# Performance work log

Measured on AMD Instinct MI355X. Metric: run time of the kernel, lower is better.

The kernel has to match this reference:

```python
import jax, jax.numpy as jnp
import numpy as np

N = 100000
E = 640000
WIDTH = 128
NUM_FEATURES = 64


def _linear_relu(h, W, b):
    # LinearBlock with batch_norm=False, dropout=0.0 -> Linear + ReLU
    return jax.nn.relu(h @ W + b)


def setup_inputs() -> dict:
    key = jax.random.key(0)
    k = jax.random.split(key, 8)
    x = jax.random.normal(k[0], (N, WIDTH), dtype=jnp.float32)
    e = jax.random.randint(k[1], (2, E), 0, N, dtype=jnp.int32)
    e_feat = jax.random.normal(k[2], (E, NUM_FEATURES), dtype=jnp.float32)
    s_e = 1.0 / np.sqrt(WIDTH + NUM_FEATURES)
    s_m = 1.0 / np.sqrt(2 * WIDTH)
    W_edge = jax.random.uniform(k[3], (WIDTH + NUM_FEATURES, WIDTH), jnp.float32, -s_e, s_e)
    b_edge = jax.random.uniform(k[4], (WIDTH,), jnp.float32, -s_e, s_e)
    W_mlp = jax.random.uniform(k[5], (2 * WIDTH, WIDTH), jnp.float32, -s_m, s_m)
    b_mlp = jax.random.uniform(k[6], (WIDTH,), jnp.float32, -s_m, s_m)
    return {"x": x, "e": e, "e_feat": e_feat, "W_edge": W_edge, "b_edge": b_edge,
            "W_mlp": W_mlp, "b_mlp": b_mlp}


def reference(x, e, e_feat, W_edge, b_edge, W_mlp, b_mlp):
    src, dst = e[0], e[1]
    diffs = x[dst] - x[src]                                   # [E, width]
    ef = diffs + _linear_relu(jnp.concatenate([diffs, e_feat], axis=1), W_edge, b_edge)
    maxes = jax.ops.segment_max(ef, dst, num_segments=x.shape[0])  # [N, width]
    # torch_scatter.scatter_max leaves empty segments at 0
    maxes = jnp.where(jnp.isneginf(maxes), 0.0, maxes)
    return x + _linear_relu(jnp.concatenate([x, maxes], axis=1), W_mlp, b_mlp)
```

## Files before the change

kernel.cpp:

```cpp
#include <hip/hip_runtime.h>
#include <hip/hip_bf16.h>
#include <limits.h>

#define NNODES 100000
#define NEDGES 640000
#define WIDTH  128
#define NFEAT  64
#define KA     192
#define KA_PAD 196
#define KB     256
#define KB_PAD 264
#define MT     64
#define STC    68
#define NB_SCAN ((NNODES + 255) / 256)
#define NB_HIST ((NEDGES + 255) / 256)
#define NB_PREP (((KA + KB) * WIDTH + 255) / 256)

typedef __attribute__((ext_vector_type(8))) short short8;
typedef __attribute__((ext_vector_type(4))) short short4v;
typedef __attribute__((ext_vector_type(4))) float floatx4;

__device__ __forceinline__ short f2bf_rne(float f) {
    unsigned u = __float_as_uint(f);
    unsigned r = u + 0x7fffu + ((u >> 16) & 1u);
    return (short)(r >> 16);
}
__device__ __forceinline__ short f2bf_t(float f) {
    return (short)(__float_as_uint(f) >> 16);
}
__device__ __forceinline__ float bf2f(short s) {
    return __uint_as_float(((unsigned)(unsigned short)s) << 16);
}
__device__ __forceinline__ unsigned encu(float f) {
    unsigned u = __float_as_uint(f);
    return (u & 0x80000000u) ? ~u : (u | 0x80000000u);
}
__device__ __forceinline__ float decu(unsigned e) {
    unsigned u = (e & 0x80000000u) ? (e ^ 0x80000000u) : ~e;
    return __uint_as_float(u);
}

__global__ __launch_bounds__(256) void prep_hist_kernel(
    const int* __restrict__ e, int* __restrict__ counts,
    const float* __restrict__ W_edge, const float* __restrict__ W_mlp,
    short* __restrict__ We_t, short* __restrict__ Wm_t)
{
    int b = blockIdx.x;
    if (b < NB_HIST) {
        int i = b * 256 + threadIdx.x;
        if (i < NEDGES) atomicAdd(&counts[e[NEDGES + i]], 1);
    } else {
        int t = (b - NB_HIST) * 256 + threadIdx.x;
        if (t < KA * WIDTH) {
            int k = t / WIDTH, n = t % WIDTH;
            We_t[n * KA + k] = f2bf_rne(W_edge[t]);
        } else if (t < (KA + KB) * WIDTH) {
            int j = t - KA * WIDTH;
            int k = j / WIDTH, n = j % WIDTH;
            Wm_t[n * KB + k] = f2bf_rne(W_mlp[j]);
        }
    }
}

__global__ __launch_bounds__(256) void scanA_kernel(
    const int* __restrict__ counts, int* __restrict__ cursor, int* __restrict__ blockSum)
{
    __shared__ int s[256];
    int tid = threadIdx.x;
    int n = blockIdx.x * 256 + tid;
    int c = (n < NNODES) ? counts[n] : 0;
    s[tid] = c;
    __syncthreads();
    for (int off = 1; off < 256; off <<= 1) {
        int v = (tid >= off) ? s[tid - off] : 0;
        __syncthreads();
        s[tid] += v;
        __syncthreads();
    }
    if (n < NNODES) cursor[n] = s[tid] - c;
    if (tid == 255) blockSum[blockIdx.x] = s[255];
}

__global__ __launch_bounds__(512) void scanB_kernel(int* __restrict__ blockSum,
                                                    int* __restrict__ blockOff)
{
    __shared__ int s[512];
    int tid = threadIdx.x;
    int c = (tid < NB_SCAN) ? blockSum[tid] : 0;
    s[tid] = c;
    __syncthreads();
    for (int off = 1; off < 512; off <<= 1) {
        int v = (tid >= off) ? s[tid - off] : 0;
        __syncthreads();
        s[tid] += v;
        __syncthreads();
    }
    if (tid < NB_SCAN) blockOff[tid] = s[tid] - c;
}

__global__ __launch_bounds__(256) void scatter_kernel(
    const int* __restrict__ e, int* __restrict__ cursor,
    const int* __restrict__ blockOff,
    uint2* __restrict__ pSD, int* __restrict__ pEid)
{
    int i = blockIdx.x * 256 + threadIdx.x;
    if (i < NEDGES) {
        int s = e[i];
        int d = e[NEDGES + i];
        int p = atomicAdd(&cursor[d], 1) + blockOff[d >> 8];
        pSD[p] = make_uint2((unsigned)s, (unsigned)d);
        pEid[p] = i;
    }
}

__global__ __launch_bounds__(256, 6) void edge_kernel(
    const float* __restrict__ x, const float* __restrict__ e_feat,
    const short* __restrict__ We_t, const float* __restrict__ b_edge,
    const uint2* __restrict__ pSD, const int* __restrict__ pEid,
    unsigned* __restrict__ mEnc)
{
    __shared__ __align__(16) short sA[MT * KA_PAD];
    __shared__ float sBias[WIDTH];
    __shared__ int   sDst[MT];
    __shared__ int   sHeadRow[MT + 1];
    __shared__ int   sMeta[3];

    const int tid = threadIdx.x;
    if (tid < WIDTH) sBias[tid] = b_edge[tid];

    const int bid = blockIdx.x;
    const int btile = (bid & 7) * (NEDGES / MT / 8) + (bid >> 3);
    const int e0 = btile * MT;

    const float4* xf4 = (const float4*)x;
    const float4* ef4 = (const float4*)e_feat;

    {
        int mq = tid >> 5, c = tid & 31;
        uint2 sd[8];
        #pragma unroll
        for (int j = 0; j < 8; ++j) sd[j] = pSD[e0 + mq + 8 * j];
        int mq2 = tid >> 4, c2 = tid & 15;
        int eid[4];
        #pragma unroll
        for (int j = 0; j < 4; ++j) eid[j] = pEid[e0 + mq2 + 16 * j];

        float4 xsA[4], xdA[4];
        #pragma unroll
        for (int j = 0; j < 4; ++j) {
            xsA[j] = xf4[(size_t)sd[j].x * 32 + c];
            xdA[j] = xf4[(size_t)sd[j].y * 32 + c];
        }
        float4 xsB[4], xdB[4];
        #pragma unroll
        for (int j = 0; j < 4; ++j) {
            xsB[j] = xf4[(size_t)sd[4 + j].x * 32 + c];
            xdB[j] = xf4[(size_t)sd[4 + j].y * 32 + c];
        }
        if (c == 0) {
            #pragma unroll
            for (int j = 0; j < 8; ++j) sDst[mq + 8 * j] = (int)sd[j].y;
        }
        #pragma unroll
        for (int j = 0; j < 4; ++j) {
            int mm = mq + 8 * j;
            short4v df;
            df.x = f2bf_t(xdA[j].x - xsA[j].x);
            df.y = f2bf_t(xdA[j].y - xsA[j].y);
            df.z = f2bf_t(xdA[j].z - xsA[j].z);
            df.w = f2bf_t(xdA[j].w - xsA[j].w);
            *(short4v*)&sA[mm * KA_PAD + c * 4] = df;
        }
        float4 fv[4];
        #pragma unroll
        for (int j = 0; j < 4; ++j) fv[j] = ef4[(size_t)eid[j] * 16 + c2];
        #pragma unroll
        for (int j = 0; j < 4; ++j) {
            int mm = mq + 8 * (4 + j);
            short4v df;
            df.x = f2bf_t(xdB[j].x - xsB[j].x);
            df.y = f2bf_t(xdB[j].y - xsB[j].y);
            df.z = f2bf_t(xdB[j].z - xsB[j].z);
            df.w = f2bf_t(xdB[j].w - xsB[j].w);
            *(short4v*)&sA[mm * KA_PAD + c * 4] = df;
        }
        #pragma unroll
        for (int j = 0; j < 4; ++j) {
            int mm = mq2 + 16 * j;
            short4v sv;
            sv.x = f2bf_t(fv[j].x); sv.y = f2bf_t(fv[j].y);
            sv.z = f2bf_t(fv[j].z); sv.w = f2bf_t(fv[j].w);
            *(short4v*)&sA[mm * KA_PAD + WIDTH + c2 * 4] = sv;
        }
    }
    __syncthreads();

    if (tid < 64) {
        bool head = (tid == 0) || (sDst[tid] != sDst[tid - 1]);
        unsigned long long mask = __ballot(head);
        int rank = __popcll(mask & ((1ull << tid) - 1ull));
        if (head) sHeadRow[rank] = tid;
        if (tid == 0) {
            int nh = (int)__popcll(mask);
            sMeta[0] = nh;
            sHeadRow[nh] = MT;
            int prevSame = 0, nextSame = 0;
            if (e0 > 0)           prevSame = (pSD[e0 - 1].y  == (unsigned)sDst[0]);
            if (e0 + MT < NEDGES) nextSame = (pSD[e0 + MT].y == (unsigned)sDst[MT - 1]);
            sMeta[1] = prevSame; sMeta[2] = nextSame;
        }
    }

    const int wave = tid >> 6;
    const int lane = tid & 63;
    const int l15  = lane & 15;
    const int kq   = (lane >> 4) << 3;
    const int quad = lane >> 4;

    floatx4 acc[4][2];
    #pragma unroll
    for (int rt = 0; rt < 4; ++rt)
        #pragma unroll
        for (int ct = 0; ct < 2; ++ct)
            acc[rt][ct] = (floatx4){0.f, 0.f, 0.f, 0.f};

    #pragma unroll
    for (int kc = 0; kc < 6; ++kc) {
        int k0 = kc * 32 + kq;
        short8 a[4];
        #pragma unroll
        for (int rt = 0; rt < 4; ++rt)
            a[rt] = *(const short8*)&sA[(rt * 16 + l15) * KA_PAD + k0];
        short8 b[2];
        #pragma unroll
        for (int ct = 0; ct < 2; ++ct)
            b[ct] = *(const short8*)&We_t[(size_t)(wave * 32 + ct * 16 + l15) * KA + k0];
        #pragma unroll
        for (int rt = 0; rt < 4; ++rt)
            #pragma unroll
            for (int ct = 0; ct < 2; ++ct)
                acc[rt][ct] = __builtin_amdgcn_mfma_f32_16x16x32_bf16(a[rt], b[ct], acc[rt][ct], 0, 0, 0);
    }

    #pragma unroll
    for (int rt = 0; rt < 4; ++rt) {
        #pragma unroll
        for (int ct = 0; ct < 2; ++ct) {
            int col = wave * 32 + ct * 16 + l15;
            float bias = sBias[col];
            #pragma unroll
            for (int i = 0; i < 4; ++i) {
                int row = rt * 16 + quad * 4 + i;
                float v = acc[rt][ct][i] + bias;
                v = v > 0.f ? v : 0.f;
                acc[rt][ct][i] = v + bf2f(sA[row * KA_PAD + col]);
            }
        }
    }
    __syncthreads();

    short* sT = sA;
    #pragma unroll
    for (int rt = 0; rt < 4; ++rt) {
        #pragma unroll
        for (int ct = 0; ct < 2; ++ct) {
            int col = wave * 32 + ct * 16 + l15;
            short4v pk;
            pk.x = f2bf_t(acc[rt][ct][0]);
            pk.y = f2bf_t(acc[rt][ct][1]);
            pk.z = f2bf_t(acc[rt][ct][2]);
            pk.w = f2bf_t(acc[rt][ct][3]);
            *(short4v*)&sT[col * STC + rt * 16 + quad * 4] = pk;
        }
    }
    __syncthreads();

    const int nh = sMeta[0], prevSame = sMeta[1], nextSame = sMeta[2];
    const unsigned* sT32 = (const unsigned*)sT;
    for (int p = tid; p < (nh << 7); p += 256) {
        int h = p >> 7, c = p & 127;
        int r0 = sHeadRow[h], r1 = sHeadRow[h + 1];
        const unsigned* colp = sT32 + c * (STC / 2);
        int w0 = r0 >> 1, w1 = (r1 - 1) >> 1;
        float m = -3.4e38f;
        for (int w = w0; w <= w1; ++w) {
            unsigned u = colp[w];
            float flo = bf2f((short)(u & 0xffffu));
            float fhi = bf2f((short)(u >> 16));
            if (2 * w >= r0)    m = fmaxf(m, flo);
            if (2 * w + 1 < r1) m = fmaxf(m, fhi);
        }
        int dst = sDst[r0];
        unsigned ev = encu(m);
        unsigned* dp = &mEnc[(size_t)dst * WIDTH + c];
        bool atom = (h == 0 && prevSame) || (h == nh - 1 && nextSame);
        if (atom) atomicMax(dp, ev);
        else      *dp = ev;
    }
}

__global__ __launch_bounds__(256) void node_kernel(
    const float* __restrict__ x, const short* __restrict__ Wm_t,
    const float* __restrict__ b_mlp, float* __restrict__ out)
{
    __shared__ short sA[MT * KB_PAD];
    __shared__ float sBias[WIDTH];

    const int tid = threadIdx.x;
    if (tid < WIDTH) sBias[tid] = b_mlp[tid];

    const int n0 = blockIdx.x * MT;
    const float4* xf4 = (const float4*)x;
    const uint4* enc4 = (const uint4*)out;

    {
        int mq = tid >> 5, c = tid & 31;
        #pragma unroll
        for (int mm = mq; mm < MT; mm += 8) {
            int node = n0 + mm;
            if (node >= NNODES) node = NNODES - 1;
            float4 xv = xf4[(size_t)node * 32 + c];
            short4v sx;
            sx.x = f2bf_rne(xv.x); sx.y = f2bf_rne(xv.y);
            sx.z = f2bf_rne(xv.z); sx.w = f2bf_rne(xv.w);
            *(short4v*)&sA[mm * KB_PAD + c * 4] = sx;
            uint4 ev = enc4[(size_t)node * 32 + c];
            short4v sm;
            sm.x = f2bf_rne(ev.x == 0u ? 0.f : decu(ev.x));
            sm.y = f2bf_rne(ev.y == 0u ? 0.f : decu(ev.y));
            sm.z = f2bf_rne(ev.z == 0u ? 0.f : decu(ev.z));
            sm.w = f2bf_rne(ev.w == 0u ? 0.f : decu(ev.w));
            *(short4v*)&sA[mm * KB_PAD + WIDTH + c * 4] = sm;
        }
    }
    __syncthreads();

    const int wave = tid >> 6;
    const int lane = tid & 63;
    const int l15  = lane & 15;
    const int kq   = (lane >> 4) << 3;
    const int quad = lane >> 4;

    floatx4 acc[4][2];
    #pragma unroll
    for (int rt = 0; rt < 4; ++rt)
        #pragma unroll
        for (int ct = 0; ct < 2; ++ct)
            acc[rt][ct] = (floatx4){0.f, 0.f, 0.f, 0.f};

    #pragma unroll
    for (int kc = 0; kc < 8; ++kc) {
        int k0 = kc * 32 + kq;
        short8 a[4];
        #pragma unroll
        for (int rt = 0; rt < 4; ++rt)
            a[rt] = *(const short8*)&sA[(rt * 16 + l15) * KB_PAD + k0];
        short8 b[2];
        #pragma unroll
        for (int ct = 0; ct < 2; ++ct)
            b[ct] = *(const short8*)&Wm_t[(size_t)(wave * 32 + ct * 16 + l15) * KB + k0];
        #pragma unroll
        for (int rt = 0; rt < 4; ++rt)
            #pragma unroll
            for (int ct = 0; ct < 2; ++ct)
                acc[rt][ct] = __builtin_amdgcn_mfma_f32_16x16x32_bf16(a[rt], b[ct], acc[rt][ct], 0, 0, 0);
    }

    #pragma unroll
    for (int rt = 0; rt < 4; ++rt) {
        #pragma unroll
        for (int ct = 0; ct < 2; ++ct) {
            int col = wave * 32 + ct * 16 + l15;
            float bias = sBias[col];
            #pragma unroll
            for (int i = 0; i < 4; ++i) {
                int row = rt * 16 + quad * 4 + i;
                int node = n0 + row;
                if (node < NNODES) {
                    float v = acc[rt][ct][i] + bias;
                    v = v > 0.f ? v : 0.f;
                    out[(size_t)node * WIDTH + col] = x[(size_t)node * WIDTH + col] + v;
                }
            }
        }
    }
}

extern "C" void kernel_launch(void* const* d_in, const int* in_sizes, int n_in,
                              void* d_out, int out_size, void* d_ws, size_t ws_size,
                              hipStream_t stream) {
    const float* x      = (const float*)d_in[0];
    const int*   e      = (const int*)d_in[1];
    const float* e_feat = (const float*)d_in[2];
    const float* W_edge = (const float*)d_in[3];
    const float* b_edge = (const float*)d_in[4];
    const float* W_mlp  = (const float*)d_in[5];
    const float* b_mlp  = (const float*)d_in[6];
    float*    out  = (float*)d_out;
    unsigned* mEnc = (unsigned*)d_out;

    short* We_t = (short*)d_ws;
    short* Wm_t = We_t + (size_t)KA * WIDTH;
    int* base     = (int*)((char*)d_ws + 114688);
    uint2* pSD    = (uint2*)base;
    int* pEid     = (int*)(base + 2 * NEDGES);
    int* counts   = pEid + NEDGES;
    int* cursor   = counts + NNODES;
    int* blockSum = cursor + NNODES;
    int* blockOff = blockSum + NB_SCAN;

    hipMemsetAsync(d_out, 0, (size_t)NNODES * WIDTH * 4, stream);
    hipMemsetAsync(counts, 0, (size_t)NNODES * 4, stream);
    prep_hist_kernel<<<NB_HIST + NB_PREP, 256, 0, stream>>>(e, counts, W_edge, W_mlp, We_t, Wm_t);
    scanA_kernel<<<NB_SCAN, 256, 0, stream>>>(counts, cursor, blockSum);
    scanB_kernel<<<1, 512, 0, stream>>>(blockSum, blockOff);
    scatter_kernel<<<(NEDGES + 255) / 256, 256, 0, stream>>>(e, cursor, blockOff, pSD, pEid);
    edge_kernel<<<NEDGES / MT, 256, 0, stream>>>(x, e_feat, We_t, b_edge, pSD, pEid, mEnc);
    node_kernel<<<(NNODES + MT - 1) / MT, 256, 0, stream>>>(x, Wm_t, b_mlp, out);
}
```

Before: 536.2 us.

## Reduce edge-kernel occupancy target, drop block swizzle, and serialize gather halves

Lowers the edge kernel's launch-bounds occupancy hint from 6 to 4 blocks per SM. It removes the XCD-style block-to-tile swizzle in favour of linear tile indexing, and restructures the x gathers into two sequential halves with fewer loads in flight. The intent is likely to give the compiler more registers and simplify addressing. The cost is less memory-level parallelism in the gather phase and different cache locality across chiplets.

```diff
diff --git a/kernel.cpp b/kernel.cpp
--- a/kernel.cpp
+++ b/kernel.cpp
@@ -113,7 +113,7 @@
     }
 }
 
-__global__ __launch_bounds__(256, 6) void edge_kernel(
+__global__ __launch_bounds__(256, 4) void edge_kernel(
     const float* __restrict__ x, const float* __restrict__ e_feat,
     const short* __restrict__ We_t, const float* __restrict__ b_edge,
     const uint2* __restrict__ pSD, const int* __restrict__ pEid,
@@ -128,10 +128,7 @@
     const int tid = threadIdx.x;
     if (tid < WIDTH) sBias[tid] = b_edge[tid];
 
-    const int bid = blockIdx.x;
-    const int btile = (bid & 7) * (NEDGES / MT / 8) + (bid >> 3);
-    const int e0 = btile * MT;
-
+    const int e0 = blockIdx.x * MT;
     const float4* xf4 = (const float4*)x;
     const float4* ef4 = (const float4*)e_feat;
 
@@ -140,50 +137,36 @@
         uint2 sd[8];
         #pragma unroll
         for (int j = 0; j < 8; ++j) sd[j] = pSD[e0 + mq + 8 * j];
+        if (c == 0) {
+            #pragma unroll
+            for (int j = 0; j < 8; ++j) sDst[mq + 8 * j] = (int)sd[j].y;
+        }
+        #pragma unroll
+        for (int half = 0; half < 2; ++half) {
+            float4 xs[4], xd[4];
+            #pragma unroll
+            for (int j = 0; j < 4; ++j) {
+                xs[j] = xf4[(size_t)sd[half * 4 + j].x * 32 + c];
+                xd[j] = xf4[(size_t)sd[half * 4 + j].y * 32 + c];
+            }
+            #pragma unroll
+            for (int j = 0; j < 4; ++j) {
+                int mm = mq + 8 * (half * 4 + j);
+                short4v df;
+                df.x = f2bf_t(xd[j].x - xs[j].x);
+                df.y = f2bf_t(xd[j].y - xs[j].y);
+                df.z = f2bf_t(xd[j].z - xs[j].z);
+                df.w = f2bf_t(xd[j].w - xs[j].w);
+                *(short4v*)&sA[mm * KA_PAD + c * 4] = df;
+            }
+        }
         int mq2 = tid >> 4, c2 = tid & 15;
         int eid[4];
         #pragma unroll
         for (int j = 0; j < 4; ++j) eid[j] = pEid[e0 + mq2 + 16 * j];
-
-        float4 xsA[4], xdA[4];
-        #pragma unroll
-        for (int j = 0; j < 4; ++j) {
-            xsA[j] = xf4[(size_t)sd[j].x * 32 + c];
-            xdA[j] = xf4[(size_t)sd[j].y * 32 + c];
-        }
-        float4 xsB[4], xdB[4];
-        #pragma unroll
-        for (int j = 0; j < 4; ++j) {
-            xsB[j] = xf4[(size_t)sd[4 + j].x * 32 + c];
-            xdB[j] = xf4[(size_t)sd[4 + j].y * 32 + c];
-        }
-        if (c == 0) {
-            #pragma unroll
-            for (int j = 0; j < 8; ++j) sDst[mq + 8 * j] = (int)sd[j].y;
-        }
-        #pragma unroll
-        for (int j = 0; j < 4; ++j) {
-            int mm = mq + 8 * j;
-            short4v df;
-            df.x = f2bf_t(xdA[j].x - xsA[j].x);
-            df.y = f2bf_t(xdA[j].y - xsA[j].y);
-            df.z = f2bf_t(xdA[j].z - xsA[j].z);
-            df.w = f2bf_t(xdA[j].w - xsA[j].w);
-            *(short4v*)&sA[mm * KA_PAD + c * 4] = df;
-        }
         float4 fv[4];
         #pragma unroll
         for (int j = 0; j < 4; ++j) fv[j] = ef4[(size_t)eid[j] * 16 + c2];
-        #pragma unroll
-        for (int j = 0; j < 4; ++j) {
-            int mm = mq + 8 * (4 + j);
-            short4v df;
-            df.x = f2bf_t(xdB[j].x - xsB[j].x);
-            df.y = f2bf_t(xdB[j].y - xsB[j].y);
-            df.z = f2bf_t(xdB[j].z - xsB[j].z);
-            df.w = f2bf_t(xdB[j].w - xsB[j].w);
-            *(short4v*)&sA[mm * KA_PAD + c * 4] = df;
-        }
         #pragma unroll
         for (int j = 0; j < 4; ++j) {
             int mm = mq2 + 16 * j;
```

Result: faster. 477.1 us (-11.0%).
